# Kernel optimization log

Measured on AMD Instinct MI355X. Metric: run time of the kernel, lower is better.

## Reference

```python
import jax, jax.numpy as jnp
import numpy as np

N_NODES = 100000
N_EDGES = 1600000
D_FEAT = 128


def sage_conv(x, src, dst, Wl, Wr, b, n_nodes):
    # gather source features, mean-aggregate at destination (PyG SAGEConv, aggr='mean')
    msgs = x[src]                                            # [E, d]
    agg_sum = jax.ops.segment_sum(msgs, dst, num_segments=n_nodes)
    cnt = jax.ops.segment_sum(jnp.ones((src.shape[0],), dtype=x.dtype), dst,
                              num_segments=n_nodes)
    mean = agg_sum / jnp.maximum(cnt, 1.0)[:, None]
    return mean @ Wl + x @ Wr + b


def setup_inputs() -> dict:
    key = jax.random.key(0)
    ks = jax.random.split(key, 9)
    def w(k, shape):
        fan_in = shape[0]
        return jax.random.normal(k, shape, dtype=jnp.float32) / np.sqrt(fan_in)
    x = jax.random.normal(ks[0], (N_NODES, D_FEAT), dtype=jnp.float32)
    edge_index = jax.random.randint(ks[1], (2, N_EDGES), 0, N_NODES, dtype=jnp.int64)
    return {
        "x": x,
        "edge_index": edge_index,
        "W1l": w(ks[2], (D_FEAT, 64)), "W1r": w(ks[3], (D_FEAT, 64)), "b1": jnp.zeros((64,), jnp.float32),
        "W2l": w(ks[4], (64, 128)),    "W2r": w(ks[5], (64, 128)),    "b2": jnp.zeros((128,), jnp.float32),
        "W3l": w(ks[6], (128, 64)),    "W3r": w(ks[7], (128, 64)),    "b3": jnp.zeros((64,), jnp.float32),
        "Wlin": w(ks[8], (64, 10)),    "blin": jnp.zeros((10,), jnp.float32),
    }


def reference(x, edge_index, W1l, W1r, b1, W2l, W2r, b2, W3l, W3r, b3, Wlin, blin):
    n = x.shape[0]
    src, dst = edge_index[0], edge_index[1]
    # dropout omitted (evaluated in inference / identity form)
    h = jnp.tanh(sage_conv(x, src, dst, W1l, W1r, b1, n))
    h = jnp.tanh(sage_conv(h, src, dst, W2l, W2r, b2, n))
    h = jnp.tanh(sage_conv(h, src, dst, W3l, W3r, b3, n))
    return h @ Wlin + blin
```

## Files before the change

kernel.cpp:

```cpp
#include <hip/hip_runtime.h>

#define THREADS 256
#define NB 256
#define NB_SHIFT 8
#define TILE_E 1024
#define EPT 2
#define BMAXPAD 512
#define WT_LD 136

typedef unsigned short ushort_t;
typedef __attribute__((ext_vector_type(8))) short bf16x8;
typedef __attribute__((ext_vector_type(4))) float f32x4;

__device__ __forceinline__ unsigned short f2bf(float f) {
    unsigned u = __float_as_uint(f);
    u += 0x7fff + ((u >> 16) & 1);
    return (unsigned short)(u >> 16);
}
__device__ __forceinline__ float bf2f(unsigned short s) {
    return __uint_as_float((unsigned)s << 16);
}
__device__ __forceinline__ float4 bf4_to_f4(ushort4 u) {
    return make_float4(bf2f(u.x), bf2f(u.y), bf2f(u.z), bf2f(u.w));
}
__device__ __forceinline__ ushort4 f4_to_bf4(float4 v) {
    ushort4 o;
    o.x = f2bf(v.x); o.y = f2bf(v.y); o.z = f2bf(v.z); o.w = f2bf(v.w);
    return o;
}
__device__ __forceinline__ unsigned pack_bf2(float a, float b) {
    return (unsigned)f2bf(a) | ((unsigned)f2bf(b) << 16);
}
__device__ __forceinline__ void acc_pair(unsigned u, float& lo, float& hi) {
    lo += __uint_as_float(u << 16);
    hi += __uint_as_float(u);
}

__global__ __launch_bounds__(64)
void detect_kernel(const unsigned* __restrict__ ei_words, int* __restrict__ flag) {
    if (threadIdx.x == 0 && blockIdx.x == 0) {
        int allzero = 1;
        for (int i = 0; i < 64; ++i) {
            if (ei_words[2 * i + 1] != 0u) { allzero = 0; break; }
        }
        *flag = allzero;
    }
}

__device__ __forceinline__ void load_edge(const void* ei, int is64, int E, int i,
                                          int& s, int& t) {
    if (is64) {
        const long long* p = (const long long*)ei;
        s = (int)p[i];
        t = (int)p[E + i];
    } else {
        const int* p = (const int*)ei;
        s = p[i];
        t = p[E + i];
    }
}

__global__ __launch_bounds__(512)
void tilesort_kernel(const void* __restrict__ ei, const int* __restrict__ flag,
                     unsigned* __restrict__ tbuf, int* __restrict__ tcnt,
                     int* __restrict__ tstart, int E, int B) {
    __shared__ int hist[BMAXPAD];
    __shared__ int wsum[8];
    const int t   = blockIdx.x;
    const int e0  = t * TILE_E;
    const int is64 = *flag;
    unsigned w[EPT];
    unsigned short bk[EPT];
    hist[threadIdx.x] = 0;
    __syncthreads();
#pragma unroll
    for (int k = 0; k < EPT; ++k) {
        const int i = e0 + k * 512 + (int)threadIdx.x;
        bk[k] = 0xFFFFu;
        w[k]  = 0u;
        if (i < E) {
            int s, d;
            load_edge(ei, is64, E, i, s, d);
            w[k]  = (unsigned)s | ((unsigned)(d & (NB - 1)) << 17);
            bk[k] = (unsigned short)(d >> NB_SHIFT);
            atomicAdd(&hist[bk[k]], 1);
        }
    }
    __syncthreads();
    const int lane = threadIdx.x & 63;
    const int wid  = threadIdx.x >> 6;
    const int v = hist[threadIdx.x];
    int incl = v;
#pragma unroll
    for (int off = 1; off < 64; off <<= 1) {
        int tt = __shfl_up(incl, off, 64);
        if (lane >= off) incl += tt;
    }
    if (lane == 63) wsum[wid] = incl;
    __syncthreads();
    int woff = 0;
    for (int ww = 0; ww < wid; ++ww) woff += wsum[ww];
    const int excl = woff + incl - v;
    hist[threadIdx.x] = excl;
    const int b = threadIdx.x;
    if (b < B) { tcnt[(size_t)t * B + b] = v; tstart[(size_t)t * B + b] = excl; }
    __syncthreads();
#pragma unroll
    for (int k = 0; k < EPT; ++k) {
        if (bk[k] != 0xFFFFu) {
            const int pos = atomicAdd(&hist[bk[k]], 1);
            tbuf[(size_t)t * TILE_E + pos] = w[k];
        }
    }
}

__global__ __launch_bounds__(256)
void transpose2_kernel(const int* __restrict__ tcnt, const int* __restrict__ tstart,
                       int* __restrict__ tcntT, int* __restrict__ tstartT,
                       int T, int B) {
    __shared__ int ta[32][33];
    __shared__ int tb[32][33];
    const int bx = blockIdx.x;
    const int by = blockIdx.y;
    const int tx = threadIdx.x & 31;
    const int ty = threadIdx.x >> 5;
#pragma unroll
    for (int r = 0; r < 4; ++r) {
        const int trow = by * 32 + ty * 4 + r;
        const int bcol = bx * 32 + tx;
        if (trow < T && bcol < B) {
            ta[ty * 4 + r][tx] = tcnt[(size_t)trow * B + bcol];
            tb[ty * 4 + r][tx] = tstart[(size_t)trow * B + bcol];
        }
    }
    __syncthreads();
#pragma unroll
    for (int r = 0; r < 4; ++r) {
        const int brow = bx * 32 + ty * 4 + r;
        const int tcol = by * 32 + tx;
        if (brow < B && tcol < T) {
            tcntT[(size_t)brow * T + tcol]   = ta[tx][ty * 4 + r];
            tstartT[(size_t)brow * T + tcol] = tb[tx][ty * 4 + r];
        }
    }
}

__global__ __launch_bounds__(256)
void scan_partial_kernel(const int* __restrict__ cnt, int* __restrict__ bsum, int n) {
    const int base = blockIdx.x * 1024;
    int v = 0;
    for (int i = threadIdx.x; i < 1024; i += 256) {
        const int idx = base + i;
        v += (idx < n) ? cnt[idx] : 0;
    }
#pragma unroll
    for (int off = 32; off > 0; off >>= 1) v += __shfl_down(v, off, 64);
    __shared__ int ws[4];
    if ((threadIdx.x & 63) == 0) ws[threadIdx.x >> 6] = v;
    __syncthreads();
    if (threadIdx.x == 0) bsum[blockIdx.x] = ws[0] + ws[1] + ws[2] + ws[3];
}

__global__ __launch_bounds__(1024)
void scan_bsum_kernel(int* __restrict__ bsum, int* __restrict__ total, int nb) {
    __shared__ int wsum[16];
    const int lane = threadIdx.x & 63;
    const int wid  = threadIdx.x >> 6;
    int run = 0;
    for (int base = 0; base < nb; base += 1024) {
        const int i = base + (int)threadIdx.x;
        const int v = (i < nb) ? bsum[i] : 0;
        int incl = v;
#pragma unroll
        for (int off = 1; off < 64; off <<= 1) {
            int t = __shfl_up(incl, off, 64);
            if (lane >= off) incl += t;
        }
        if (lane == 63) wsum[wid] = incl;
        __syncthreads();
        if (wid == 0) {
            int wv = (lane < 16) ? wsum[lane] : 0;
#pragma unroll
            for (int off = 1; off < 16; off <<= 1) {
                int t = __shfl_up(wv, off, 64);
                if (lane >= off) wv += t;
            }
            if (lane < 16) wsum[lane] = wv;
        }
        __syncthreads();
        const int wbase = (wid > 0) ? wsum[wid - 1] : 0;
        const int tot   = wsum[15];
        if (i < nb) bsum[i] = run + wbase + incl - v;
        run += tot;
        __syncthreads();
    }
    if (threadIdx.x == 0) *total = run;
}

__global__ __launch_bounds__(256)
void scan_final_kernel(const int* __restrict__ cnt, const int* __restrict__ bsum,
                       int* __restrict__ outp, int n) {
    const int base = blockIdx.x * 1024 + threadIdx.x * 4;
    int a0 = 0, a1 = 0, a2 = 0, a3 = 0;
    if (base + 0 < n) a0 = cnt[base + 0];
    if (base + 1 < n) a1 = cnt[base + 1];
    if (base + 2 < n) a2 = cnt[base + 2];
    if (base + 3 < n) a3 = cnt[base + 3];
    const int mysum = a0 + a1 + a2 + a3;
    const int lane = threadIdx.x & 63;
    const int wid  = threadIdx.x >> 6;
    int incl = mysum;
#pragma unroll
    for (int off = 1; off < 64; off <<= 1) {
        int t = __shfl_up(incl, off, 64);
        if (lane >= off) incl += t;
    }
    __shared__ int ws[4];
    if (lane == 63) ws[wid] = incl;
    __syncthreads();
    int woff = 0;
    for (int w = 0; w < wid; ++w) woff += ws[w];
    int pre = bsum[blockIdx.x] + woff + (incl - mysum);
    if (base + 0 < n) outp[base + 0] = pre; pre += a0;
    if (base + 1 < n) outp[base + 1] = pre; pre += a1;
    if (base + 2 < n) outp[base + 2] = pre; pre += a2;
    if (base + 3 < n) outp[base + 3] = pre;
}

__global__ __launch_bounds__(512)
void finesort_kernel(const unsigned* __restrict__ tbuf, const int* __restrict__ tcntT,
                     const int* __restrict__ tstartT, const int* __restrict__ hbase,
                     int* __restrict__ rowptr, int* __restrict__ esrc,
                     int n, int E, int T, int B) {
    __shared__ int hist[NB];
    __shared__ int wsum[4];
    const int b  = blockIdx.x;
    const int e0 = hbase[(size_t)b * T];
    if (threadIdx.x < NB) hist[threadIdx.x] = 0;
    __syncthreads();
    for (int t = threadIdx.x; t < T; t += 512) {
        const int c  = tcntT[(size_t)b * T + t];
        const int ls = tstartT[(size_t)b * T + t];
        const unsigned* __restrict__ src = tbuf + (size_t)t * TILE_E + ls;
        for (int k = 0; k < c; ++k) atomicAdd(&hist[src[k] >> 17], 1);
    }
    __syncthreads();
    if (threadIdx.x < NB) {
        const int lane = threadIdx.x & 63;
        const int wid  = threadIdx.x >> 6;
        const int v = hist[threadIdx.x];
        int incl = v;
#pragma unroll
        for (int off = 1; off < 64; off <<= 1) {
            int tt = __shfl_up(incl, off, 64);
            if (lane >= off) incl += tt;
        }
        if (lane == 63) wsum[wid] = incl;
    }
    __syncthreads();
    if (threadIdx.x < NB) {
        const int wid = threadIdx.x >> 6;
        const int v   = hist[threadIdx.x];
        const int lane = threadIdx.x & 63;
        int incl = v;
#pragma unroll
        for (int off = 1; off < 64; off <<= 1) {
            int tt = __shfl_up(incl, off, 64);
            if (lane >= off) incl += tt;
        }
        int woff = 0;
        for (int w = 0; w < wid; ++w) woff += wsum[w];
        const int excl = woff + incl - v;
        hist[threadIdx.x] = e0 + excl;
        const int node = b * NB + (int)threadIdx.x;
        if (node < n) rowptr[node] = e0 + excl;
    }
    if (b == 0 && threadIdx.x == 0) rowptr[n] = E;
    __syncthreads();
    for (int t = threadIdx.x; t < T; t += 512) {
        const int c  = tcntT[(size_t)b * T + t];
        const int ls = tstartT[(size_t)b * T + t];
        const unsigned* __restrict__ src = tbuf + (size_t)t * TILE_E + ls;
        for (int k = 0; k < c; ++k) {
            const unsigned wv = src[k];
            const int pos = atomicAdd(&hist[wv >> 17], 1);
            esrc[pos] = (int)((wv & 0x1FFFFu) << 7);
        }
    }
}

__global__ __launch_bounds__(256)
void pack_dual_kernel(const float* __restrict__ Wl, const float* __restrict__ Wr,
                      ushort_t* __restrict__ WT) {
    int i = blockIdx.x * 256 + threadIdx.x;
    if (i >= 128 * 128) return;
    int k = i >> 7, c = i & 127;
    float v = (c < 64) ? Wl[k * 64 + c] : Wr[k * 64 + (c - 64)];
    WT[c * WT_LD + k] = f2bf(v);
}
__global__ __launch_bounds__(256)
void pack_stack_kernel(const float* __restrict__ Wl, const float* __restrict__ Wr,
                       ushort_t* __restrict__ WT) {
    int i = blockIdx.x * 256 + threadIdx.x;
    if (i >= 128 * 128) return;
    int k = i >> 7, c = i & 127;
    float v = (k < 64) ? Wl[k * 128 + c] : Wr[(k - 64) * 128 + c];
    WT[c * WT_LD + k] = f2bf(v);
}

template <int AMODE, bool TANH_BIAS, bool OUT_SPLIT>
__global__ __launch_bounds__(256)
void mfma_gemm_kernel(const void* __restrict__ Av1, const void* __restrict__ Av2,
                      const ushort_t* __restrict__ WT, const float* __restrict__ bias,
                      ushort_t* __restrict__ C1, ushort_t* __restrict__ C2, int n) {
    __shared__ ushort_t sW[128 * WT_LD];
    {
        const uint4* gsrc = (const uint4*)WT;
        uint4* ldst = (uint4*)sW;
        for (int i = threadIdx.x; i < 128 * WT_LD * 2 / 16; i += 256) ldst[i] = gsrc[i];
    }
    __syncthreads();
    const int lane = threadIdx.x & 63;
    const int wave = threadIdx.x >> 6;
    const int kg   = lane >> 4;
    const int row0 = blockIdx.x * 64 + wave * 16;
    const int rA   = min(row0 + (lane & 15), n - 1);

    bf16x8 a[4];
    if (AMODE == 0) {
        const float* A = (const float*)Av1;
#pragma unroll
        for (int t = 0; t < 4; ++t) {
            const float4 lo = *(const float4*)(A + (size_t)rA * 128 + t * 32 + kg * 8);
            const float4 hi = *(const float4*)(A + (size_t)rA * 128 + t * 32 + kg * 8 + 4);
            const ushort4 u0 = f4_to_bf4(lo), u1 = f4_to_bf4(hi);
            bf16x8 av;
            av[0] = (short)u0.x; av[1] = (short)u0.y; av[2] = (short)u0.z; av[3] = (short)u0.w;
            av[4] = (short)u1.x; av[5] = (short)u1.y; av[6] = (short)u1.z; av[7] = (short)u1.w;
            a[t] = av;
        }
    } else if (AMODE == 1) {
        const ushort_t* A1 = (const ushort_t*)Av1;
        const ushort_t* A2 = (const ushort_t*)Av2;
        a[0] = *(const bf16x8*)(A1 + (size_t)rA * 64 + 0 + kg * 8);
        a[1] = *(const bf16x8*)(A1 + (size_t)rA * 64 + 32 + kg * 8);
        a[2] = *(const bf16x8*)(A2 + (size_t)rA * 64 + 0 + kg * 8);
        a[3] = *(const bf16x8*)(A2 + (size_t)rA * 64 + 32 + kg * 8);
    } else {
        const ushort_t* A = (const ushort_t*)Av1;
#pragma unroll
        for (int t = 0; t < 4; ++t)
            a[t] = *(const bf16x8*)(A + (size_t)rA * 128 + t * 32 + kg * 8);
    }

    f32x4 acc[8];
#pragma unroll
    for (int ct = 0; ct < 8; ++ct) acc[ct] = (f32x4)(0.f);

#pragma unroll
    for (int ct = 0; ct < 8; ++ct) {
        const int c0 = ct * 16 + (lane & 15);
#pragma unroll
        for (int t = 0; t < 4; ++t) {
            const bf16x8 b = *(const bf16x8*)(sW + (size_t)c0 * WT_LD + t * 32 + kg * 8);
            acc[ct] = __builtin_amdgcn_mfma_f32_16x16x32_bf16(b, a[t], acc[ct], 0, 0, 0);
        }
    }

    const int r = row0 + (lane & 15);
    if (r < n) {
#pragma unroll
        for (int ct = 0; ct < 8; ++ct) {
            float v0 = acc[ct][0], v1 = acc[ct][1], v2 = acc[ct][2], v3 = acc[ct][3];
            if (TANH_BIAS) {
                const float4 bv = *(const float4*)(bias + ct * 16 + kg * 4);
                v0 = tanhf(v0 + bv.x); v1 = tanhf(v1 + bv.y);
                v2 = tanhf(v2 + bv.z); v3 = tanhf(v3 + bv.w);
            }
            uint2 pk;
            pk.x = pack_bf2(v0, v1);
            pk.y = pack_bf2(v2, v3);
            if (OUT_SPLIT) {
                if (ct < 4)
                    *(uint2*)(C1 + (size_t)r * 64 + kg * 4 + ct * 16) = pk;
                else
                    *(uint2*)(C2 + (size_t)r * 64 + kg * 4 + (ct - 4) * 16) = pk;
            } else {
                *(uint2*)(C1 + (size_t)r * 128 + kg * 4 + ct * 16) = pk;
            }
        }
    }
}

template <int MODE>
__global__ __launch_bounds__(THREADS)
void gather_fuse_kernel(const int* __restrict__ rowptr, const int* __restrict__ esrc,
                        const ushort_t* __restrict__ p, const ushort_t* __restrict__ q,
                        const float* __restrict__ bias, ushort_t* __restrict__ h1out,
                        const float* __restrict__ Wlin, const float* __restrict__ blin,
                        float* __restrict__ out, int n) {
    constexpr int CH  = 16;
    constexpr int NPB = THREADS / CH;
    const int node = blockIdx.x * NPB + (int)(threadIdx.x / CH);
    const int c    = threadIdx.x & (CH - 1);
    if (node >= n) return;
    const int begin = rowptr[node];
    const int end   = rowptr[node + 1];
    const char* __restrict__ base = (const char*)p + 8 * c;
    float ax = 0.f, ay = 0.f, az = 0.f, aw = 0.f;
    int e = begin;
    for (; e + 8 <= end; e += 8) {
        uint2 d[8];
#pragma unroll
        for (int j = 0; j < 8; ++j) d[j] = *(const uint2*)(base + esrc[e + j]);
#pragma unroll
        for (int j = 0; j < 8; ++j) { acc_pair(d[j].x, ax, ay); acc_pair(d[j].y, az, aw); }
    }
    if (e + 4 <= end) {
        uint2 d[4];
#pragma unroll
        for (int j = 0; j < 4; ++j) d[j] = *(const uint2*)(base + esrc[e + j]);
#pragma unroll
        for (int j = 0; j < 4; ++j) { acc_pair(d[j].x, ax, ay); acc_pair(d[j].y, az, aw); }
        e += 4;
    }
    for (; e < end; ++e) {
        const uint2 d = *(const uint2*)(base + esrc[e]);
        acc_pair(d.x, ax, ay); acc_pair(d.y, az, aw);
    }
    const float inv = 1.0f / fmaxf((float)(end - begin), 1.0f);
    const float4 qv = bf4_to_f4(*(const ushort4*)(q + (size_t)node * 64 + 4 * c));
    const float4 bv = *(const float4*)(bias + 4 * c);
    float4 o;
    o.x = tanhf(ax * inv + qv.x + bv.x);
    o.y = tanhf(ay * inv + qv.y + bv.y);
    o.z = tanhf(az * inv + qv.z + bv.z);
    o.w = tanhf(aw * inv + qv.w + bv.w);
    if (MODE == 0) {
        *(ushort4*)(h1out + (size_t)node * 64 + 4 * c) = f4_to_bf4(o);
    } else {
        float tot[10];
        const float* __restrict__ w0 = Wlin + (4 * c + 0) * 10;
        const float* __restrict__ w1 = Wlin + (4 * c + 1) * 10;
        const float* __restrict__ w2 = Wlin + (4 * c + 2) * 10;
        const float* __restrict__ w3 = Wlin + (4 * c + 3) * 10;
#pragma unroll
        for (int j = 0; j < 10; ++j)
            tot[j] = o.x * w0[j] + o.y * w1[j] + o.z * w2[j] + o.w * w3[j];
#pragma unroll
        for (int m = 1; m < 16; m <<= 1) {
#pragma unroll
            for (int j = 0; j < 10; ++j) tot[j] += __shfl_xor(tot[j], m, 64);
        }
        if (c == 0) {
            float* orow = out + (size_t)node * 10;
#pragma unroll
            for (int j = 0; j < 10; ++j) orow[j] = tot[j] + blin[j];
        }
    }
}

__global__ __launch_bounds__(THREADS)
void gather_mean_kernel(const int* __restrict__ rowptr, const int* __restrict__ esrc,
                        const ushort_t* __restrict__ h1, ushort_t* __restrict__ agg,
                        int n) {
    constexpr int CH  = 16;
    constexpr int NPB = THREADS / CH;
    const int node = blockIdx.x * NPB + (int)(threadIdx.x / CH);
    const int c    = threadIdx.x & (CH - 1);
    if (node >= n) return;
    const int begin = rowptr[node];
    const int end   = rowptr[node + 1];
    const char* __restrict__ base = (const char*)h1 + 8 * c;
    float ax = 0.f, ay = 0.f, az = 0.f, aw = 0.f;
    int e = begin;
    for (; e + 8 <= end; e += 8) {
        uint2 d[8];
#pragma unroll
        for (int j = 0; j < 8; ++j) d[j] = *(const uint2*)(base + esrc[e + j]);
#pragma unroll
        for (int j = 0; j < 8; ++j) { acc_pair(d[j].x, ax, ay); acc_pair(d[j].y, az, aw); }
    }
    if (e + 4 <= end) {
        uint2 d[4];
#pragma unroll
        for (int j = 0; j < 4; ++j) d[j] = *(const uint2*)(base + esrc[e + j]);
#pragma unroll
        for (int j = 0; j < 4; ++j) { acc_pair(d[j].x, ax, ay); acc_pair(d[j].y, az, aw); }
        e += 4;
    }
    for (; e < end; ++e) {
        const uint2 d = *(const uint2*)(base + esrc[e]);
        acc_pair(d.x, ax, ay); acc_pair(d.y, az, aw);
    }
    const float inv = 1.0f / fmaxf((float)(end - begin), 1.0f);
    ushort4 o = f4_to_bf4(make_float4(ax * inv, ay * inv, az * inv, aw * inv));
    *(ushort4*)(agg + (size_t)node * 64 + 4 * c) = o;
}

extern "C" void kernel_launch(void* const* d_in, const int* in_sizes, int n_in,
                              void* d_out, int out_size, void* d_ws, size_t ws_size,
                              hipStream_t stream) {
    const float* x    = (const float*)d_in[0];
    const void*  ei   = d_in[1];
    const float* W1l  = (const float*)d_in[2];
    const float* W1r  = (const float*)d_in[3];
    const float* b1   = (const float*)d_in[4];
    const float* W2l  = (const float*)d_in[5];
    const float* W2r  = (const float*)d_in[6];
    const float* b2   = (const float*)d_in[7];
    const float* W3l  = (const float*)d_in[8];
    const float* W3r  = (const float*)d_in[9];
    const float* b3   = (const float*)d_in[10];
    const float* Wlin = (const float*)d_in[11];
    const float* blin = (const float*)d_in[12];
    float* out = (float*)d_out;

    const int n = in_sizes[0] / 128;
    const int E = in_sizes[1] / 2;
    const int B = (n + NB - 1) / NB;
    const int T = (E + TILE_E - 1) / TILE_E;
    const int Ctot = B * T;

    char* ws = (char*)d_ws;
    size_t off = 0;
    auto carve = [&](size_t bytes) {
        void* p = ws + off;
        off += (bytes + 255) & ~(size_t)255;
        return p;
    };
    int*      flag    = (int*)     carve(256);
    int*      bsum    = (int*)     carve(8192);
    unsigned* tbuf    = (unsigned*)carve((size_t)T * TILE_E * 4);
    int*      tcnt    = (int*)     carve((size_t)Ctot * 4);
    int*      tstart  = (int*)     carve((size_t)Ctot * 4);
    int*      tcntT   = (int*)     carve((size_t)Ctot * 4);
    int*      tstartT = (int*)     carve((size_t)Ctot * 4);
    int*      hbase   = (int*)     carve((size_t)(Ctot + 1) * 4);
    int*      rowptr  = (int*)     carve((size_t)(n + 1) * 4);
    int*      esrc    = (int*)     carve((size_t)E * 4);
    ushort_t* WT1     = (ushort_t*)carve((size_t)128 * WT_LD * 2);
    ushort_t* WT2     = (ushort_t*)carve((size_t)128 * WT_LD * 2);
    ushort_t* WT3     = (ushort_t*)carve((size_t)128 * WT_LD * 2);
    ushort_t* p       = (ushort_t*)carve((size_t)n * 64 * 2);
    ushort_t* q       = (ushort_t*)carve((size_t)n * 64 * 2);
    ushort_t* h1      = (ushort_t*)carve((size_t)n * 64 * 2);
    ushort_t* agg     = (ushort_t*)carve((size_t)n * 64 * 2);
    ushort_t* h2      = (ushort_t*)carve((size_t)n * 128 * 2);
    (void)ws_size;

    const int cscan   = (Ctot + 1023) / 1024;
    const int gblocks = (n + 63) / 64;

    pack_dual_kernel <<<64, 256, 0, stream>>>(W1l, W1r, WT1);
    pack_stack_kernel<<<64, 256, 0, stream>>>(W2l, W2r, WT2);
    pack_dual_kernel <<<64, 256, 0, stream>>>(W3l, W3r, WT3);

    detect_kernel<<<1, 64, 0, stream>>>((const unsigned*)ei, flag);
    tilesort_kernel<<<T, 512, 0, stream>>>(ei, flag, tbuf, tcnt, tstart, E, B);
    {
        dim3 tg((B + 31) / 32, (T + 31) / 32);
        transpose2_kernel<<<tg, 256, 0, stream>>>(tcnt, tstart, tcntT, tstartT, T, B);
    }
    scan_partial_kernel<<<cscan, 256, 0, stream>>>(tcntT, bsum, Ctot);
    scan_bsum_kernel<<<1, 1024, 0, stream>>>(bsum, hbase + Ctot, cscan);
    scan_final_kernel<<<cscan, 256, 0, stream>>>(tcntT, bsum, hbase, Ctot);
    finesort_kernel<<<B, 512, 0, stream>>>(tbuf, tcntT, tstartT, hbase,
                                           rowptr, esrc, n, E, T, B);

    mfma_gemm_kernel<0, false, true><<<gblocks, 256, 0, stream>>>(
        x, nullptr, WT1, nullptr, p, q, n);
    gather_fuse_kernel<0><<<(n + 15) / 16, THREADS, 0, stream>>>(
        rowptr, esrc, p, q, b1, h1, nullptr, nullptr, nullptr, n);

    gather_mean_kernel<<<(n + 15) / 16, THREADS, 0, stream>>>(rowptr, esrc, h1, agg, n);
    mfma_gemm_kernel<1, true, false><<<gblocks, 256, 0, stream>>>(
        agg, h1, WT2, b2, h2, nullptr, n);

    mfma_gemm_kernel<2, false, true><<<gblocks, 256, 0, stream>>>(
        h2, nullptr, WT3, nullptr, p, q, n);
    gather_fuse_kernel<1><<<(n + 15) / 16, THREADS, 0, stream>>>(
        rowptr, esrc, p, q, b3, nullptr, Wlin, blin, out, n);
}
```

Baseline: 244.9 us.

## Sub-sort edges by source slice within each node; cache Wlin in LDS

The fine sort now keys each edge by destination node plus a 3-bit slice of its source index, so each node's edge list comes out grouped by source region. Later gathers should then touch memory with better locality. The gather loops drop the 8-wide unroll in favour of a simpler 4-wide loop. The final fused kernel stages Wlin and blin in shared memory instead of reading them from global memory. In exchange the sort uses a histogram eight times larger with a 4-per-thread scan, and the smaller unroll gives fewer loads in flight per thread.

New measurement: 248.4 us. Within noise of the previous version (+1.4%).

```diff
diff --git a/kernel.cpp b/kernel.cpp
--- a/kernel.cpp
+++ b/kernel.cpp
@@ -7,6 +7,8 @@
 #define EPT 2
 #define BMAXPAD 512
 #define WT_LD 136
+#define SLICE_SHIFT 14
+#define KEYS (NB * 8)
 
 typedef unsigned short ushort_t;
 typedef __attribute__((ext_vector_type(8))) short bf16x8;
@@ -232,50 +234,11 @@
                      const int* __restrict__ tstartT, const int* __restrict__ hbase,
                      int* __restrict__ rowptr, int* __restrict__ esrc,
                      int n, int E, int T, int B) {
-    __shared__ int hist[NB];
-    __shared__ int wsum[4];
+    __shared__ int hist[KEYS];
+    __shared__ int wsum[8];
     const int b  = blockIdx.x;
     const int e0 = hbase[(size_t)b * T];
-    if (threadIdx.x < NB) hist[threadIdx.x] = 0;
-    __syncthreads();
-    for (int t = threadIdx.x; t < T; t += 512) {
-        const int c  = tcntT[(size_t)b * T + t];
-        const int ls = tstartT[(size_t)b * T + t];
-        const unsigned* __restrict__ src = tbuf + (size_t)t * TILE_E + ls;
-        for (int k = 0; k < c; ++k) atomicAdd(&hist[src[k] >> 17], 1);
-    }
-    __syncthreads();
-    if (threadIdx.x < NB) {
-        const int lane = threadIdx.x & 63;
-        const int wid  = threadIdx.x >> 6;
-        const int v = hist[threadIdx.x];
-        int incl = v;
-#pragma unroll
-        for (int off = 1; off < 64; off <<= 1) {
-            int tt = __shfl_up(incl, off, 64);
-            if (lane >= off) incl += tt;
-        }
-        if (lane == 63) wsum[wid] = incl;
-    }
-    __syncthreads();
-    if (threadIdx.x < NB) {
-        const int wid = threadIdx.x >> 6;
-        const int v   = hist[threadIdx.x];
-        const int lane = threadIdx.x & 63;
-        int incl = v;
-#pragma unroll
-        for (int off = 1; off < 64; off <<= 1) {
-            int tt = __shfl_up(incl, off, 64);
-            if (lane >= off) incl += tt;
-        }
-        int woff = 0;
-        for (int w = 0; w < wid; ++w) woff += wsum[w];
-        const int excl = woff + incl - v;
-        hist[threadIdx.x] = e0 + excl;
-        const int node = b * NB + (int)threadIdx.x;
-        if (node < n) rowptr[node] = e0 + excl;
-    }
-    if (b == 0 && threadIdx.x == 0) rowptr[n] = E;
+    for (int i = threadIdx.x; i < KEYS; i += 512) hist[i] = 0;
     __syncthreads();
     for (int t = threadIdx.x; t < T; t += 512) {
         const int c  = tcntT[(size_t)b * T + t];
@@ -283,8 +246,53 @@
         const unsigned* __restrict__ src = tbuf + (size_t)t * TILE_E + ls;
         for (int k = 0; k < c; ++k) {
             const unsigned wv = src[k];
-            const int pos = atomicAdd(&hist[wv >> 17], 1);
-            esrc[pos] = (int)((wv & 0x1FFFFu) << 7);
+            const int key = ((int)(wv >> 17) << 3) | (int)((wv & 0x1FFFFu) >> SLICE_SHIFT);
+            atomicAdd(&hist[key], 1);
+        }
+    }
+    __syncthreads();
+    const int base4 = (int)threadIdx.x * 4;
+    const int a0 = hist[base4 + 0];
+    const int a1 = hist[base4 + 1];
+    const int a2 = hist[base4 + 2];
+    const int a3 = hist[base4 + 3];
+    const int mysum = a0 + a1 + a2 + a3;
+    const int lane = threadIdx.x & 63;
+    const int wid  = threadIdx.x >> 6;
+    int incl = mysum;
+#pragma unroll
+    for (int off = 1; off < 64; off <<= 1) {
+        int tt = __shfl_up(incl, off, 64);
+        if (lane >= off) incl += tt;
+    }
+    if (lane == 63) wsum[wid] = incl;
+    __syncthreads();
+    int woff = 0;
+    for (int w = 0; w < wid; ++w) woff += wsum[w];
+    int pre = woff + incl - mysum;
+#pragma unroll
+    for (int r = 0; r < 4; ++r) {
+        const int k = base4 + r;
+        const int a = (r == 0) ? a0 : (r == 1) ? a1 : (r == 2) ? a2 : a3;
+        hist[k] = e0 + pre;
+        if ((k & 7) == 0) {
+            const int node = b * NB + (k >> 3);
+            if (node < n) rowptr[node] = e0 + pre;
+        }
+        pre += a;
+    }
+    if (b == 0 && threadIdx.x == 0) rowptr[n] = E;
+    __syncthreads();
+    for (int t = threadIdx.x; t < T; t += 512) {
+        const int c  = tcntT[(size_t)b * T + t];
+        const int ls = tstartT[(size_t)b * T + t];
+        const unsigned* __restrict__ src = tbuf + (size_t)t * TILE_E + ls;
+        for (int k = 0; k < c; ++k) {
+            const unsigned wv = src[k];
+            const unsigned s = wv & 0x1FFFFu;
+            const int key = ((int)(wv >> 17) << 3) | (int)(s >> SLICE_SHIFT);
+            const int pos = atomicAdd(&hist[key], 1);
+            esrc[pos] = (int)(s << 7);
         }
     }
 }
@@ -401,6 +409,13 @@
                         float* __restrict__ out, int n) {
     constexpr int CH  = 16;
     constexpr int NPB = THREADS / CH;
+    __shared__ float sW[MODE == 1 ? 640 : 1];
+    __shared__ float sb[MODE == 1 ? 10 : 1];
+    if (MODE == 1) {
+        for (int i = threadIdx.x; i < 640; i += THREADS) sW[i] = Wlin[i];
+        if (threadIdx.x < 10) sb[threadIdx.x] = blin[threadIdx.x];
+        __syncthreads();
+    }
     const int node = blockIdx.x * NPB + (int)(threadIdx.x / CH);
     const int c    = threadIdx.x & (CH - 1);
     if (node >= n) return;
@@ -409,20 +424,16 @@
     const char* __restrict__ base = (const char*)p + 8 * c;
     float ax = 0.f, ay = 0.f, az = 0.f, aw = 0.f;
     int e = begin;
-    for (; e + 8 <= end; e += 8) {
-        uint2 d[8];
-#pragma unroll
-        for (int j = 0; j < 8; ++j) d[j] = *(const uint2*)(base + esrc[e + j]);
-#pragma unroll
-        for (int j = 0; j < 8; ++j) { acc_pair(d[j].x, ax, ay); acc_pair(d[j].y, az, aw); }
-    }
-    if (e + 4 <= end) {
-        uint2 d[4];
-#pragma unroll
-        for (int j = 0; j < 4; ++j) d[j] = *(const uint2*)(base + esrc[e + j]);
-#pragma unroll
-        for (int j = 0; j < 4; ++j) { acc_pair(d[j].x, ax, ay); acc_pair(d[j].y, az, aw); }
-        e += 4;
+    for (; e + 4 <= end; e += 4) {
+        const int o0 = esrc[e + 0], o1 = esrc[e + 1], o2 = esrc[e + 2], o3 = esrc[e + 3];
+        const uint2 d0 = *(const uint2*)(base + o0);
+        const uint2 d1 = *(const uint2*)(base + o1);
+        const uint2 d2 = *(const uint2*)(base + o2);
+        const uint2 d3 = *(const uint2*)(base + o3);
+        acc_pair(d0.x, ax, ay); acc_pair(d0.y, az, aw);
+        acc_pair(d1.x, ax, ay); acc_pair(d1.y, az, aw);
+        acc_pair(d2.x, ax, ay); acc_pair(d2.y, az, aw);
+        acc_pair(d3.x, ax, ay); acc_pair(d3.y, az, aw);
     }
     for (; e < end; ++e) {
         const uint2 d = *(const uint2*)(base + esrc[e]);
@@ -440,10 +451,10 @@
         *(ushort4*)(h1out + (size_t)node * 64 + 4 * c) = f4_to_bf4(o);
     } else {
         float tot[10];
-        const float* __restrict__ w0 = Wlin + (4 * c + 0) * 10;
-        const float* __restrict__ w1 = Wlin + (4 * c + 1) * 10;
-        const float* __restrict__ w2 = Wlin + (4 * c + 2) * 10;
-        const float* __restrict__ w3 = Wlin + (4 * c + 3) * 10;
+        const float* __restrict__ w0 = sW + (4 * c + 0) * 10;
+        const float* __restrict__ w1 = sW + (4 * c + 1) * 10;
+        const float* __restrict__ w2 = sW + (4 * c + 2) * 10;
+        const float* __restrict__ w3 = sW + (4 * c + 3) * 10;
 #pragma unroll
         for (int j = 0; j < 10; ++j)
             tot[j] = o.x * w0[j] + o.y * w1[j] + o.z * w2[j] + o.w * w3[j];
@@ -455,7 +466,7 @@
         if (c == 0) {
             float* orow = out + (size_t)node * 10;
 #pragma unroll
-            for (int j = 0; j < 10; ++j) orow[j] = tot[j] + blin[j];
+            for (int j = 0; j < 10; ++j) orow[j] = tot[j] + sb[j];
         }
     }
 }
@@ -474,20 +485,16 @@
     const char* __restrict__ base = (const char*)h1 + 8 * c;
     float ax = 0.f, ay = 0.f, az = 0.f, aw = 0.f;
     int e = begin;
-    for (; e + 8 <= end; e += 8) {
-        uint2 d[8];
-#pragma unroll
-        for (int j = 0; j < 8; ++j) d[j] = *(const uint2*)(base + esrc[e + j]);
-#pragma unroll
-        for (int j = 0; j < 8; ++j) { acc_pair(d[j].x, ax, ay); acc_pair(d[j].y, az, aw); }
-    }
-    if (e + 4 <= end) {
-        uint2 d[4];
-#pragma unroll
-        for (int j = 0; j < 4; ++j) d[j] = *(const uint2*)(base + esrc[e + j]);
-#pragma unroll
-        for (int j = 0; j < 4; ++j) { acc_pair(d[j].x, ax, ay); acc_pair(d[j].y, az, aw); }
-        e += 4;
+    for (; e + 4 <= end; e += 4) {
+        const int o0 = esrc[e + 0], o1 = esrc[e + 1], o2 = esrc[e + 2], o3 = esrc[e + 3];
+        const uint2 d0 = *(const uint2*)(base + o0);
+        const uint2 d1 = *(const uint2*)(base + o1);
+        const uint2 d2 = *(const uint2*)(base + o2);
+        const uint2 d3 = *(const uint2*)(base + o3);
+        acc_pair(d0.x, ax, ay); acc_pair(d0.y, az, aw);
+        acc_pair(d1.x, ax, ay); acc_pair(d1.y, az, aw);
+        acc_pair(d2.x, ax, ay); acc_pair(d2.y, az, aw);
+        acc_pair(d3.x, ax, ay); acc_pair(d3.y, az, aw);
     }
     for (; e < end; ++e) {
         const uint2 d = *(const uint2*)(base + esrc[e]);
```
